# Kernel optimization log

Measured on AMD Instinct MI355X. Metric: run time of the kernel, lower is better.

The kernel has to match this reference:

```python
import jax, jax.numpy as jnp
import numpy as np

R_, RD_, D_, C_ = 4, 64, 256, 64   # num_relations, relation_dim, input_dim, max_chains
B_, T_ = 32, 512
OUT = R_ * RD_                      # output_dim = num_relations * relation_dim
EPS = 1e-100                        # underflows to 0 in fp32, same as torch


def setup_inputs() -> dict:
    key = jax.random.key(0)
    ks = jax.random.split(key, 10)
    X = jax.random.normal(ks[0], (B_, T_, D_), jnp.float32)
    M = jax.random.randint(ks[1], (B_, T_), 0, 2, jnp.int32)
    Ei = jax.random.randint(ks[2], (B_, T_, C_), 0, 2, jnp.int32)
    Eo = jax.random.randint(ks[3], (B_, T_, C_), 0, 2, jnp.int32)
    Ri = jax.random.randint(ks[4], (B_, T_, C_), 0, R_, jnp.int32)
    Ro = jax.random.randint(ks[5], (B_, T_, C_), 0, R_, jnp.int32)
    W = jax.random.normal(ks[6], (D_, OUT), jnp.float32) * np.sqrt(6.0 / (D_ + OUT))
    U = jax.random.normal(ks[7], (OUT, OUT), jnp.float32) * np.sqrt(6.0 / (OUT + OUT))
    b = jnp.zeros((OUT,), jnp.float32)
    Watt = jax.random.normal(ks[8], (R_, D_), jnp.float32) * 0.1
    return dict(X=X, M=M, Ei=Ei, Eo=Eo, Ri=Ri, Ro=Ro, W=W, U=U, b=b, Watt=Watt)


def _forward(X, M, Ei, Eo, Ri, Ro, W, U, b, Watt):
    B = X.shape[0]
    dt = X.dtype
    # All three gates share the same W/U/b in the original module.
    Wstk = jnp.concatenate([W, W, W], axis=1)   # [D, 3*OUT]
    Ustk = jnp.concatenate([U, U, U], axis=1)   # [OUT, 3*OUT]

    # time-major
    Xre = jnp.transpose(X, (1, 0, 2))           # [T,B,D]
    Xpre = jnp.einsum('tbd,de->tbe', Xre, Wstk) # [T,B,3*OUT] precomputed input proj
    Mre = jnp.transpose(M, (1, 0))              # [T,B]
    Eire = jnp.transpose(Ei, (1, 0, 2))         # [T,B,C]
    Eore = jnp.transpose(Eo, (1, 0, 2))
    Rire = jnp.transpose(Ri, (1, 0, 2))
    Rore = jnp.transpose(Ro, (1, 0, 2))

    h0 = jnp.zeros((B, OUT), dt)
    m0 = jnp.zeros((B, C_, RD_), dt)

    def step(carry, inp):
        hprev, mprev = carry
        x, xp, m, ei, eo, ri, ro = inp
        # gather: one-hot over relations for each chain slot
        r1 = jax.nn.one_hot(ri, R_, dtype=dt)                 # [B,C,R]
        # attention over chains
        v = jnp.einsum('bcr,rd->bcd', r1, Watt)               # [B,C,D]
        actvs = jnp.einsum('bcd,bd->bc', v, x)                # [B,C]
        e = ei.astype(dt)
        am = jnp.exp(actvs) * e + EPS
        alphas = am / jnp.sum(am, axis=1, keepdims=True)      # [B,C]
        agg = jnp.transpose(alphas[:, :, None] * r1, (0, 2, 1))  # [B,R,C]
        prev = jnp.einsum('brc,bcd->brd', agg, mprev).reshape(B, OUT)  # [B,OUT]
        agg_out = jnp.sum(agg, axis=2)                        # [B,R]
        # fused GRU cell (shared weights across gates)
        h2h = prev @ Ustk                                     # [B,3*OUT]
        xr, xz, xh = xp[:, :OUT], xp[:, OUT:2 * OUT], xp[:, 2 * OUT:]
        hr, hz, hh = h2h[:, :OUT], h2h[:, OUT:2 * OUT], h2h[:, 2 * OUT:]
        rg = jax.nn.sigmoid(xr + hr + b)
        z = jax.nn.sigmoid(xz + hz + b)
        ht = jnp.tanh(xh + rg * hh + b)
        hnew = (1.0 - z) * prev + z * ht                      # [B,OUT]
        # scatter new hidden state back into per-chain memory
        hnew_r = hnew.reshape(B, R_, RD_)
        ro1 = jax.nn.one_hot(ro, R_, dtype=dt)                # [B,C,R]
        mnew = jnp.einsum('bcr,brd->bcd', ro1, hnew_r)        # [B,C,RD]
        mflt = m.astype(dt)[:, None]                          # [B,1]
        hout = (1.0 - mflt) * hprev + mflt * hnew
        eo_r = (mflt * eo.astype(dt))[:, :, None]             # [B,C,1]
        mout = (1.0 - eo_r) * mprev + eo_r * mnew
        return (hout, mout), (hout, mout, agg_out)

    _, (outs, mems, aggs) = jax.lax.scan(
        step, (h0, m0), (Xre, Xpre, Mre, Eire, Eore, Rire, Rore))
    return (jnp.transpose(outs, (1, 0, 2)),        # [B,T,OUT]
            jnp.transpose(mems, (1, 0, 2, 3)),     # [B,T,C,RD]
            jnp.transpose(aggs, (1, 0, 2)))        # [B,T,R]


def reference(X, M, Ei, Eo, Ri, Ro, W, U, b, Watt):
    return _forward(X, M, Ei, Eo, Ri, Ro, W, U, b, Watt)
```

## Files before the change

### kernel.cpp

```cpp
#include <hip/hip_runtime.h>

#define B_   32
#define T_   512
#define D_   256
#define C_   64
#define R_   4
#define RD_  64
#define OUT_ 256

__device__ __forceinline__ void bar_lds() {
  asm volatile("s_waitcnt lgkmcnt(0)" ::: "memory");
  __builtin_amdgcn_s_barrier();
  asm volatile("" ::: "memory");
}

template <int CTRL>
__device__ __forceinline__ float dpp_add(float v) {
  int s = __builtin_amdgcn_update_dpp(0, __float_as_int(v), CTRL, 0xF, 0xF, true);
  return v + __int_as_float(s);
}
__device__ __forceinline__ float row16_sum(float v) {
  v = dpp_add<0xB1>(v);
  v = dpp_add<0x4E>(v);
  v = dpp_add<0x141>(v);
  v = dpp_add<0x140>(v);
  return v;
}
__device__ __forceinline__ float rlane(float v, int l) {
  return __int_as_float(__builtin_amdgcn_readlane(__float_as_int(v), l));
}
__device__ __forceinline__ int rlane_i(int v, int l) {
  return __builtin_amdgcn_readlane(v, l);
}
__device__ __forceinline__ float wave_sum_dpp(float v) {
  const float r = row16_sum(v);
  return (rlane(r, 0) + rlane(r, 16)) + (rlane(r, 32) + rlane(r, 48));
}

__global__ __launch_bounds__(256) void xpre_kernel(const float* __restrict__ X,
                                                   const float* __restrict__ W,
                                                   float* __restrict__ XP) {
  __shared__ __align__(16) float xs[32][D_];
  const int j = threadIdx.x;
  const int row0 = blockIdx.x * 32;
  for (int k = 0; k < 32; ++k)
    xs[k][j] = X[(size_t)(row0 + k) * D_ + j];
  __syncthreads();
  float acc[32];
#pragma unroll
  for (int k = 0; k < 32; ++k) acc[k] = 0.f;
  for (int d4 = 0; d4 < D_ / 4; ++d4) {
    const float w0 = W[(d4 * 4 + 0) * OUT_ + j];
    const float w1 = W[(d4 * 4 + 1) * OUT_ + j];
    const float w2 = W[(d4 * 4 + 2) * OUT_ + j];
    const float w3 = W[(d4 * 4 + 3) * OUT_ + j];
#pragma unroll
    for (int k = 0; k < 32; ++k) {
      const float4 x4 = *(const float4*)&xs[k][d4 * 4];
      acc[k] = fmaf(x4.x, w0, fmaf(x4.y, w1, fmaf(x4.z, w2, fmaf(x4.w, w3, acc[k]))));
    }
  }
  for (int k = 0; k < 32; ++k)
    XP[(size_t)(row0 + k) * OUT_ + j] = acc[k];
}

__global__ __launch_bounds__(256) void attnK(const float* __restrict__ X,
                                             const int* __restrict__ Ri,
                                             const int* __restrict__ Ei,
                                             const float* __restrict__ Watt,
                                             float* __restrict__ walG,
                                             float* __restrict__ aggs) {
  const int wv = threadIdx.x >> 6;
  const int lane = threadIdx.x & 63;
  const size_t bt = (size_t)blockIdx.x * 4 + wv;
  const int r4 = lane >> 4, seg = lane & 15;

  float y = 0.f;
#pragma unroll
  for (int q = 0; q < 4; ++q) {
    const float4 wt = *(const float4*)&Watt[(r4 << 8) + (seg << 4) + (q << 2)];
    const float4 xv = *(const float4*)&X[bt * D_ + (seg << 4) + (q << 2)];
    y = fmaf(xv.x, wt.x, y);
    y = fmaf(xv.y, wt.y, y);
    y = fmaf(xv.z, wt.z, y);
    y = fmaf(xv.w, wt.w, y);
  }
  y = row16_sum(y);
  const float y0 = rlane(y, 0), y1 = rlane(y, 16);
  const float y2 = rlane(y, 32), y3 = rlane(y, 48);
  const int ric = Ri[bt * C_ + lane];
  const float eic = (float)Ei[bt * C_ + lane];
  float yv = (ric & 1) ? y1 : y0;
  const float yw = (ric & 1) ? y3 : y2;
  yv = (ric & 2) ? yw : yv;
  const float am = __expf(yv) * eic;
  const float tot = wave_sum_dpp(am);
  const float alpha = __fdividef(am, tot);

  const float w0 = (ric == 0) ? alpha : 0.f;
  const float w1 = (ric == 1) ? alpha : 0.f;
  const float w2 = (ric == 2) ? alpha : 0.f;
  const float w3 = (ric == 3) ? alpha : 0.f;
  walG[bt * 256 + 0 * C_ + lane] = w0;
  walG[bt * 256 + 1 * C_ + lane] = w1;
  walG[bt * 256 + 2 * C_ + lane] = w2;
  walG[bt * 256 + 3 * C_ + lane] = w3;
  const float s0 = wave_sum_dpp(w0);
  const float s1 = wave_sum_dpp(w1);
  const float s2 = wave_sum_dpp(w2);
  const float s3 = wave_sum_dpp(w3);
  if (lane == 0) {
    float4 v = {s0, s1, s2, s3};
    *(float4*)&aggs[bt * R_] = v;
  }
}

__global__ __launch_bounds__(1024, 4) void gruA(
    const int* __restrict__ M, const int* __restrict__ Eo,
    const int* __restrict__ Ro, const float* __restrict__ U,
    const float* __restrict__ Bv, const float* __restrict__ XP,
    const float* __restrict__ walG, float* __restrict__ outs) {
  __shared__ __align__(16) float shp[16][256];
  __shared__ __align__(16) float pBred[16][256];
  __shared__ __align__(16) float shprev[OUT_];
  __shared__ __align__(16) float sh_hnew[OUT_];
  __shared__ int sh_tl[T_];
  __shared__ int sh_nT;

  const int tid = threadIdx.x;
  const int lane = tid & 63;
  const int w = tid >> 6;
  const int b = blockIdx.x;
  const size_t bt0 = (size_t)b * T_;

  float ureg[64];
#pragma unroll
  for (int jj = 0; jj < 4; ++jj)
#pragma unroll
    for (int i = 0; i < 16; ++i)
      ureg[(jj << 4) + i] = U[(size_t)((w << 4) + i) * OUT_ + (jj << 6) + lane];
  const float breg = Bv[tid & 255];

  float mtreg[4];
#pragma unroll
  for (int q = 0; q < 4; ++q) mtreg[q] = 0.f;

  if (tid < 64) {
    int base = 0;
    for (int ch = 0; ch < 8; ++ch) {
      const int mv = M[bt0 + (ch << 6) + lane];
      const unsigned long long mask = __ballot(mv != 0);
      if (mv) {
        const unsigned long long lt = ((lane == 63) ? ~0ull : ((1ull << (lane + 1)) - 1)) >> 1;
        sh_tl[base + __popcll(mask & lt)] = (ch << 6) + lane;
      }
      base += __popcll(mask);
    }
    if (lane == 0) sh_nT = base;
  }
  __syncthreads();
  const int nT = sh_nT;

  {
    const int t0 = (nT > 0) ? sh_tl[0] : T_;
    const int j = tid & 255;
    for (int t = tid >> 8; t < t0; t += 4)
      outs[(bt0 + t) * OUT_ + j] = 0.f;
  }
  if (nT == 0) return;

  const int cwal = (w << 2) + (lane >> 4);
  const int rwal = lane & 3;
  const int croeo = (w << 2) + (lane & 3);
  float walS0 = 0.f, xpS0 = 0.f, walS1 = 0.f, xpS1 = 0.f;
  int reS0 = 0, reS1 = 0;
  {
    const int t0 = sh_tl[0];
    walS0 = walG[(bt0 + t0) * 256 + (rwal << 6) + cwal];
    if (w < 4) xpS0 = XP[(bt0 + t0) * 256 + tid];
    reS0 = Ro[(bt0 + t0) * C_ + croeo] | (Eo[(bt0 + t0) * C_ + croeo] << 8);
  }
  if (nT > 1) {
    const int t1 = sh_tl[1];
    walS1 = walG[(bt0 + t1) * 256 + (rwal << 6) + cwal];
    if (w < 4) xpS1 = XP[(bt0 + t1) * 256 + tid];
    reS1 = Ro[(bt0 + t1) * C_ + croeo] | (Eo[(bt0 + t1) * C_ + croeo] << 8);
  }

  auto do_step = [&](int k, float& walS, float& xpS, int& reS) {
    const int tk = sh_tl[k];
    const size_t bt = bt0 + tk;
    const int reC = reS;

    float a0 = 0.f, a1 = 0.f, a2 = 0.f, a3 = 0.f;
#pragma unroll
    for (int q = 0; q < 4; ++q) {
      const float mq = mtreg[q];
      a0 = fmaf(rlane(walS, (q << 4) + 0), mq, a0);
      a1 = fmaf(rlane(walS, (q << 4) + 1), mq, a1);
      a2 = fmaf(rlane(walS, (q << 4) + 2), mq, a2);
      a3 = fmaf(rlane(walS, (q << 4) + 3), mq, a3);
    }
    shp[w][0 * 64 + lane] = a0;
    shp[w][1 * 64 + lane] = a1;
    shp[w][2 * 64 + lane] = a2;
    shp[w][3 * 64 + lane] = a3;
    bar_lds();

    const int kidx = (w << 4) + (lane & 15);
    float px = 0.f;
#pragma unroll
    for (int sw = 0; sw < 16; sw += 4) {
      const float t0 = shp[sw + 0][kidx], t1 = shp[sw + 1][kidx];
      const float t2 = shp[sw + 2][kidx], t3 = shp[sw + 3][kidx];
      px += (t0 + t1) + (t2 + t3);
    }
    if (lane < 16) shprev[kidx] = px;
    float p0 = 0.f, p1 = 0.f, p2 = 0.f, p3 = 0.f;
#pragma unroll
    for (int i = 0; i < 16; ++i) {
      const float pk = rlane(px, i);
      p0 = fmaf(pk, ureg[i], p0);
      p1 = fmaf(pk, ureg[16 + i], p1);
      p2 = fmaf(pk, ureg[32 + i], p2);
      p3 = fmaf(pk, ureg[48 + i], p3);
    }
    pBred[w][0 * 64 + lane] = p0;
    pBred[w][1 * 64 + lane] = p1;
    pBred[w][2 * 64 + lane] = p2;
    pBred[w][3 * 64 + lane] = p3;
    bar_lds();

    if (w < 4) {
      float h2h = 0.f;
#pragma unroll
      for (int kw = 0; kw < 16; kw += 4) {
        const float t0 = pBred[kw + 0][tid], t1 = pBred[kw + 1][tid];
        const float t2 = pBred[kw + 2][tid], t3 = pBred[kw + 3][tid];
        h2h += (t0 + t1) + (t2 + t3);
      }
      const float pOwn = shprev[tid];
      const float g1 = xpS + h2h + breg;
      const float rg = 1.f / (1.f + __expf(-g1));
      const float targ = xpS + rg * h2h + breg;
      const float e2 = __expf(2.f * targ);
      const float ht = 1.f - 2.f / (e2 + 1.f);
      const float hn = (1.f - rg) * pOwn + rg * ht;
      sh_hnew[tid] = hn;
      outs[bt * OUT_ + tid] = hn;
    }
    if (k + 2 < nT) {
      const int t2 = sh_tl[k + 2];
      walS = walG[(bt0 + t2) * 256 + (rwal << 6) + cwal];
      if (w < 4) xpS = XP[(bt0 + t2) * 256 + tid];
      reS = Ro[(bt0 + t2) * C_ + croeo] | (Eo[(bt0 + t2) * C_ + croeo] << 8);
    }
    bar_lds();

    const float h0 = sh_hnew[0 * 64 + lane];
    const float h1 = sh_hnew[1 * 64 + lane];
    const float h2 = sh_hnew[2 * 64 + lane];
    const float h3 = sh_hnew[3 * 64 + lane];
#pragma unroll
    for (int q = 0; q < 4; ++q) {
      const int re = rlane_i(reC, q);
      const int ro = re & 0xFF;
      const float ha = (ro & 1) ? h1 : h0;
      const float hb = (ro & 1) ? h3 : h2;
      const float hs = (ro & 2) ? hb : ha;
      mtreg[q] = (re & 0x100) ? hs : mtreg[q];
    }
    if (w >= 8) {
      const int idx = tid - 512;
      const int rr = idx >> 8;
      const int j = idx & 255;
      const int tnext = (k + 1 < nT) ? sh_tl[k + 1] : T_;
      const float hv = sh_hnew[j];
      for (int t = tk + 1 + rr; t < tnext; t += 2)
        outs[(bt0 + t) * OUT_ + j] = hv;
    }
  };

  for (int k = 0; k < nT; k += 2) {
    do_step(k, walS0, xpS0, reS0);
    if (k + 1 < nT) do_step(k + 1, walS1, xpS1, reS1);
  }
}

__global__ __launch_bounds__(512) void memsB(const int* __restrict__ M,
                                             const int* __restrict__ Eo,
                                             const int* __restrict__ Ro,
                                             const float* __restrict__ hbuf,
                                             float* __restrict__ mems) {
  __shared__ int lastA[T_];
  const int tid = threadIdx.x;
  const int b = blockIdx.x >> 6;
  const int c = blockIdx.x & 63;
  const size_t bt0 = (size_t)b * T_;
  {
    const int upd = M[bt0 + tid] & Eo[(bt0 + tid) * C_ + c];
    lastA[tid] = upd ? tid : -1;
  }
  __syncthreads();
  for (int off = 1; off < T_; off <<= 1) {
    const int u = (tid >= off) ? lastA[tid - off] : -1;
    const int v = lastA[tid];
    __syncthreads();
    lastA[tid] = (u > v) ? u : v;
    __syncthreads();
  }
  const int d = tid & 63;
  const int t8 = tid >> 6;
  for (int tt = 0; tt < 64; ++tt) {
    const int t = (tt << 3) + t8;
    const int tau = lastA[t];
    float v = 0.f;
    if (tau >= 0) {
      const int rc = Ro[(bt0 + tau) * C_ + c];
      v = hbuf[(bt0 + tau) * OUT_ + (rc << 6) + d];
    }
    mems[((bt0 + t) * C_ + c) * RD_ + d] = v;
  }
}

extern "C" void kernel_launch(void* const* d_in, const int* in_sizes, int n_in,
                              void* d_out, int out_size, void* d_ws, size_t ws_size,
                              hipStream_t stream) {
  const float* X = (const float*)d_in[0];
  const int* M = (const int*)d_in[1];
  const int* Ei = (const int*)d_in[2];
  const int* Eo = (const int*)d_in[3];
  const int* Ri = (const int*)d_in[4];
  const int* Ro = (const int*)d_in[5];
  const float* W = (const float*)d_in[6];
  const float* U = (const float*)d_in[7];
  const float* Bv = (const float*)d_in[8];
  const float* Watt = (const float*)d_in[9];

  float* outs = (float*)d_out;
  float* mems = outs + (size_t)B_ * T_ * OUT_;
  float* aggs = mems + (size_t)B_ * T_ * C_ * RD_;
  float* XP = (float*)d_ws;
  float* walG = mems;

  xpre_kernel<<<dim3(B_ * T_ / 32), dim3(256), 0, stream>>>(X, W, XP);
  attnK<<<dim3(B_ * T_ / 4), dim3(256), 0, stream>>>(X, Ri, Ei, Watt, walG, aggs);
  gruA<<<dim3(B_), dim3(1024), 0, stream>>>(M, Eo, Ro, U, Bv, XP, walG, outs);
  memsB<<<dim3(B_ * C_), dim3(512), 0, stream>>>(M, Eo, Ro, outs, mems);
}
```

Before: 730.0 us.

## Precompute next step's chain aggregation a step ahead to cut one barrier

Restructures the serial GRU recurrence so the attention-weighted chain aggregation for the next step is computed one step early into a double-buffered LDS array. Chains that the current step's hidden state is about to overwrite are handled by a small correction: waves 4-7 build per-relation coefficients and these are applied to the new hidden state. The aim is to remove one of the three block barriers per timestep from the critical path. The trade-off is extra register pressure, more prefetched loads and more complex index logic. The fill of repeated outputs is also moved before the barrier, with a tail loop after the main loop.

```diff
diff --git a/kernel.cpp b/kernel.cpp
--- a/kernel.cpp
+++ b/kernel.cpp
@@ -120,10 +120,11 @@
     const int* __restrict__ Ro, const float* __restrict__ U,
     const float* __restrict__ Bv, const float* __restrict__ XP,
     const float* __restrict__ walG, float* __restrict__ outs) {
-  __shared__ __align__(16) float shp[16][256];
+  __shared__ __align__(16) float shp2[2][16][256];
   __shared__ __align__(16) float pBred[16][256];
   __shared__ __align__(16) float shprev[OUT_];
   __shared__ __align__(16) float sh_hnew[OUT_];
+  __shared__ float sh_coef[16];
   __shared__ int sh_tl[T_];
   __shared__ int sh_nT;
 
@@ -158,6 +159,9 @@
     }
     if (lane == 0) sh_nT = base;
   }
+  for (int i = tid; i < 16 * 256; i += 1024) ((float*)shp2[0])[i] = 0.f;
+  if (tid < 256) sh_hnew[tid] = 0.f;
+  if (tid < 16) sh_coef[tid] = 0.f;
   __syncthreads();
   const int nT = sh_nT;
 
@@ -172,63 +176,111 @@
   const int cwal = (w << 2) + (lane >> 4);
   const int rwal = lane & 3;
   const int croeo = (w << 2) + (lane & 3);
-  float walS0 = 0.f, xpS0 = 0.f, walS1 = 0.f, xpS1 = 0.f;
-  int reS0 = 0, reS1 = 0;
-  {
-    const int t0 = sh_tl[0];
-    walS0 = walG[(bt0 + t0) * 256 + (rwal << 6) + cwal];
-    if (w < 4) xpS0 = XP[(bt0 + t0) * 256 + tid];
-    reS0 = Ro[(bt0 + t0) * C_ + croeo] | (Eo[(bt0 + t0) * C_ + croeo] << 8);
-  }
-  if (nT > 1) {
-    const int t1 = sh_tl[1];
-    walS1 = walG[(bt0 + t1) * 256 + (rwal << 6) + cwal];
-    if (w < 4) xpS1 = XP[(bt0 + t1) * 256 + tid];
-    reS1 = Ro[(bt0 + t1) * C_ + croeo] | (Eo[(bt0 + t1) * C_ + croeo] << 8);
-  }
-
-  auto do_step = [&](int k, float& walS, float& xpS, int& reS) {
+
+  auto loadWalS = [&](int t) { return walG[(bt0 + t) * 256 + (rwal << 6) + cwal]; };
+  auto loadRe = [&](int t) { return Ro[(bt0 + t) * C_ + croeo] | (Eo[(bt0 + t) * C_ + croeo] << 8); };
+  auto loadReF = [&](int t) { return Ro[(bt0 + t) * C_ + lane] | (Eo[(bt0 + t) * C_ + lane] << 8); };
+  auto loadWalC = [&](int t) {
+    float4 v;
+    v.x = walG[(bt0 + t) * 256 + 0 * 64 + lane];
+    v.y = walG[(bt0 + t) * 256 + 1 * 64 + lane];
+    v.z = walG[(bt0 + t) * 256 + 2 * 64 + lane];
+    v.w = walG[(bt0 + t) * 256 + 3 * 64 + lane];
+    return v;
+  };
+
+  const int tl0 = sh_tl[0];
+  const int tl1 = sh_tl[(nT > 1) ? 1 : 0];
+  const int tl2 = sh_tl[(nT > 2) ? 2 : (nT - 1)];
+  float walS0 = loadWalS(tl1), walS1 = loadWalS(tl2);
+  float xpS0 = (w < 4) ? XP[(bt0 + tl0) * 256 + tid] : 0.f;
+  float xpS1 = (w < 4) ? XP[(bt0 + tl1) * 256 + tid] : 0.f;
+  int reS0 = loadRe(tl0), reS1 = loadRe(tl1);
+  float4 walC0 = loadWalC(tl1), walC1 = loadWalC(tl2);
+  int reF0 = loadReF(tl0), reF1 = loadReF(tl1);
+  int rePrev = 0;
+
+  auto do_step = [&](int k, float& walS, float& xpS, int& reS, float4& walC,
+                     int& reF) {
+    const int cur = k & 1, nxt = cur ^ 1;
     const int tk = sh_tl[k];
     const size_t bt = bt0 + tk;
-    const int reC = reS;
-
-    float a0 = 0.f, a1 = 0.f, a2 = 0.f, a3 = 0.f;
-#pragma unroll
-    for (int q = 0; q < 4; ++q) {
-      const float mq = mtreg[q];
-      a0 = fmaf(rlane(walS, (q << 4) + 0), mq, a0);
-      a1 = fmaf(rlane(walS, (q << 4) + 1), mq, a1);
-      a2 = fmaf(rlane(walS, (q << 4) + 2), mq, a2);
-      a3 = fmaf(rlane(walS, (q << 4) + 3), mq, a3);
-    }
-    shp[w][0 * 64 + lane] = a0;
-    shp[w][1 * 64 + lane] = a1;
-    shp[w][2 * 64 + lane] = a2;
-    shp[w][3 * 64 + lane] = a3;
-    bar_lds();
-
+
+    {
+      const float h0 = sh_hnew[lane];
+      const float h1 = sh_hnew[64 + lane];
+      const float h2 = sh_hnew[128 + lane];
+      const float h3 = sh_hnew[192 + lane];
+#pragma unroll
+      for (int q = 0; q < 4; ++q) {
+        const int re = rlane_i(rePrev, q);
+        const int ro = re & 0xFF;
+        const float ha = (ro & 1) ? h1 : h0;
+        const float hb = (ro & 1) ? h3 : h2;
+        const float hs = (ro & 2) ? hb : ha;
+        mtreg[q] = (re & 0x100) ? hs : mtreg[q];
+      }
+    }
+    {
+      float a0 = 0.f, a1 = 0.f, a2 = 0.f, a3 = 0.f;
+#pragma unroll
+      for (int q = 0; q < 4; ++q) {
+        const int re = rlane_i(reS, q);
+        const float mq = (re & 0x100) ? 0.f : mtreg[q];
+        a0 = fmaf(rlane(walS, (q << 4) + 0), mq, a0);
+        a1 = fmaf(rlane(walS, (q << 4) + 1), mq, a1);
+        a2 = fmaf(rlane(walS, (q << 4) + 2), mq, a2);
+        a3 = fmaf(rlane(walS, (q << 4) + 3), mq, a3);
+      }
+      shp2[nxt][w][0 * 64 + lane] = a0;
+      shp2[nxt][w][1 * 64 + lane] = a1;
+      shp2[nxt][w][2 * 64 + lane] = a2;
+      shp2[nxt][w][3 * 64 + lane] = a3;
+    }
     const int kidx = (w << 4) + (lane & 15);
+    const int rI = w >> 2, d = kidx & 63;
     float px = 0.f;
 #pragma unroll
     for (int sw = 0; sw < 16; sw += 4) {
-      const float t0 = shp[sw + 0][kidx], t1 = shp[sw + 1][kidx];
-      const float t2 = shp[sw + 2][kidx], t3 = shp[sw + 3][kidx];
+      const float t0 = shp2[cur][sw + 0][kidx], t1 = shp2[cur][sw + 1][kidx];
+      const float t2 = shp2[cur][sw + 2][kidx], t3 = shp2[cur][sw + 3][kidx];
       px += (t0 + t1) + (t2 + t3);
     }
+    {
+      const float c0 = sh_coef[(rI << 2) + 0];
+      const float c1 = sh_coef[(rI << 2) + 1];
+      const float c2 = sh_coef[(rI << 2) + 2];
+      const float c3 = sh_coef[(rI << 2) + 3];
+      px = fmaf(c0, sh_hnew[d], px);
+      px = fmaf(c1, sh_hnew[64 + d], px);
+      px = fmaf(c2, sh_hnew[128 + d], px);
+      px = fmaf(c3, sh_hnew[192 + d], px);
+    }
     if (lane < 16) shprev[kidx] = px;
-    float p0 = 0.f, p1 = 0.f, p2 = 0.f, p3 = 0.f;
-#pragma unroll
-    for (int i = 0; i < 16; ++i) {
-      const float pk = rlane(px, i);
-      p0 = fmaf(pk, ureg[i], p0);
-      p1 = fmaf(pk, ureg[16 + i], p1);
-      p2 = fmaf(pk, ureg[32 + i], p2);
-      p3 = fmaf(pk, ureg[48 + i], p3);
-    }
-    pBred[w][0 * 64 + lane] = p0;
-    pBred[w][1 * 64 + lane] = p1;
-    pBred[w][2 * 64 + lane] = p2;
-    pBred[w][3 * 64 + lane] = p3;
+    {
+      float p0 = 0.f, p1 = 0.f, p2 = 0.f, p3 = 0.f;
+#pragma unroll
+      for (int i = 0; i < 16; ++i) {
+        const float pk = rlane(px, i);
+        p0 = fmaf(pk, ureg[i], p0);
+        p1 = fmaf(pk, ureg[16 + i], p1);
+        p2 = fmaf(pk, ureg[32 + i], p2);
+        p3 = fmaf(pk, ureg[48 + i], p3);
+      }
+      pBred[w][0 * 64 + lane] = p0;
+      pBred[w][1 * 64 + lane] = p1;
+      pBred[w][2 * 64 + lane] = p2;
+      pBred[w][3 * 64 + lane] = p3;
+    }
+    if (w >= 8 && k > 0) {
+      const int idx = tid - 512;
+      const int rr = idx >> 8;
+      const int j = idx & 255;
+      const int tprev = sh_tl[k - 1];
+      const float hv = sh_hnew[j];
+      for (int t = tprev + 1 + rr; t < tk; t += 2)
+        outs[(bt0 + t) * OUT_ + j] = hv;
+    }
     bar_lds();
 
     if (w < 4) {
@@ -248,42 +300,47 @@
       const float hn = (1.f - rg) * pOwn + rg * ht;
       sh_hnew[tid] = hn;
       outs[bt * OUT_ + tid] = hn;
-    }
-    if (k + 2 < nT) {
-      const int t2 = sh_tl[k + 2];
-      walS = walG[(bt0 + t2) * 256 + (rwal << 6) + cwal];
-      if (w < 4) xpS = XP[(bt0 + t2) * 256 + tid];
-      reS = Ro[(bt0 + t2) * C_ + croeo] | (Eo[(bt0 + t2) * C_ + croeo] << 8);
+    } else if (w < 8) {
+      const int r2 = w - 4;
+      const float mask =
+          (((reF >> 8) & 1) && ((reF & 0xFF) == r2)) ? 1.f : 0.f;
+      const float s0 = wave_sum_dpp(walC.x * mask);
+      const float s1 = wave_sum_dpp(walC.y * mask);
+      const float s2 = wave_sum_dpp(walC.z * mask);
+      const float s3 = wave_sum_dpp(walC.w * mask);
+      if (lane == 0) {
+        sh_coef[0 * 4 + r2] = s0;
+        sh_coef[1 * 4 + r2] = s1;
+        sh_coef[2 * 4 + r2] = s2;
+        sh_coef[3 * 4 + r2] = s3;
+      }
+    }
+    rePrev = reS;
+    {
+      const int k2 = (k + 2 < nT) ? k + 2 : nT - 1;
+      const int k3 = (k + 3 < nT) ? k + 3 : nT - 1;
+      const int t2v = sh_tl[k2], t3v = sh_tl[k3];
+      walS = loadWalS(t3v);
+      if (w < 4) xpS = XP[(bt0 + t2v) * 256 + tid];
+      reS = loadRe(t2v);
+      walC = loadWalC(t3v);
+      reF = loadReF(t2v);
     }
     bar_lds();
-
-    const float h0 = sh_hnew[0 * 64 + lane];
-    const float h1 = sh_hnew[1 * 64 + lane];
-    const float h2 = sh_hnew[2 * 64 + lane];
-    const float h3 = sh_hnew[3 * 64 + lane];
-#pragma unroll
-    for (int q = 0; q < 4; ++q) {
-      const int re = rlane_i(reC, q);
-      const int ro = re & 0xFF;
-      const float ha = (ro & 1) ? h1 : h0;
-      const float hb = (ro & 1) ? h3 : h2;
-      const float hs = (ro & 2) ? hb : ha;
-      mtreg[q] = (re & 0x100) ? hs : mtreg[q];
-    }
-    if (w >= 8) {
-      const int idx = tid - 512;
-      const int rr = idx >> 8;
-      const int j = idx & 255;
-      const int tnext = (k + 1 < nT) ? sh_tl[k + 1] : T_;
-      const float hv = sh_hnew[j];
-      for (int t = tk + 1 + rr; t < tnext; t += 2)
-        outs[(bt0 + t) * OUT_ + j] = hv;
-    }
   };
 
   for (int k = 0; k < nT; k += 2) {
-    do_step(k, walS0, xpS0, reS0);
-    if (k + 1 < nT) do_step(k + 1, walS1, xpS1, reS1);
+    do_step(k, walS0, xpS0, reS0, walC0, reF0);
+    if (k + 1 < nT)
+      do_step(k + 1, walS1, xpS1, reS1, walC1, reF1);
+  }
+
+  {
+    const int tlast = sh_tl[nT - 1];
+    const int j = tid & 255;
+    const float hv = sh_hnew[j];
+    for (int t = tlast + 1 + (tid >> 8); t < T_; t += 4)
+      outs[(bt0 + t) * OUT_ + j] = hv;
   }
 }
 
```

Measured after the change: 798.9 us. 1.09x slower.

## Fuse prep kernels and write per-chain memory directly from GRU kernel

Applied to the files above, without the earlier changes.

Merges the input projection and attention kernels into one launch that branches on block index. When the workspace is large enough, attention weights move to the workspace and the GRU kernel writes the mems output itself while it runs, so the separate memsB pass that re-read the hidden states is dropped. This removes one or two launches and a large re-read, but adds many serial global stores inside the 32-block recurrent kernel, which could lengthen its critical path.

```diff
diff --git a/kernel.cpp b/kernel.cpp
--- a/kernel.cpp
+++ b/kernel.cpp
@@ -37,81 +37,79 @@
   return (rlane(r, 0) + rlane(r, 16)) + (rlane(r, 32) + rlane(r, 48));
 }
 
-__global__ __launch_bounds__(256) void xpre_kernel(const float* __restrict__ X,
-                                                   const float* __restrict__ W,
-                                                   float* __restrict__ XP) {
+__global__ __launch_bounds__(256) void prepK(
+    const float* __restrict__ X, const float* __restrict__ W,
+    const int* __restrict__ Ri, const int* __restrict__ Ei,
+    const float* __restrict__ Watt, float* __restrict__ XP,
+    float* __restrict__ walG, float* __restrict__ aggs) {
   __shared__ __align__(16) float xs[32][D_];
-  const int j = threadIdx.x;
-  const int row0 = blockIdx.x * 32;
-  for (int k = 0; k < 32; ++k)
-    xs[k][j] = X[(size_t)(row0 + k) * D_ + j];
-  __syncthreads();
-  float acc[32];
-#pragma unroll
-  for (int k = 0; k < 32; ++k) acc[k] = 0.f;
-  for (int d4 = 0; d4 < D_ / 4; ++d4) {
-    const float w0 = W[(d4 * 4 + 0) * OUT_ + j];
-    const float w1 = W[(d4 * 4 + 1) * OUT_ + j];
-    const float w2 = W[(d4 * 4 + 2) * OUT_ + j];
-    const float w3 = W[(d4 * 4 + 3) * OUT_ + j];
-#pragma unroll
-    for (int k = 0; k < 32; ++k) {
-      const float4 x4 = *(const float4*)&xs[k][d4 * 4];
-      acc[k] = fmaf(x4.x, w0, fmaf(x4.y, w1, fmaf(x4.z, w2, fmaf(x4.w, w3, acc[k]))));
-    }
-  }
-  for (int k = 0; k < 32; ++k)
-    XP[(size_t)(row0 + k) * OUT_ + j] = acc[k];
-}
-
-__global__ __launch_bounds__(256) void attnK(const float* __restrict__ X,
-                                             const int* __restrict__ Ri,
-                                             const int* __restrict__ Ei,
-                                             const float* __restrict__ Watt,
-                                             float* __restrict__ walG,
-                                             float* __restrict__ aggs) {
-  const int wv = threadIdx.x >> 6;
-  const int lane = threadIdx.x & 63;
-  const size_t bt = (size_t)blockIdx.x * 4 + wv;
-  const int r4 = lane >> 4, seg = lane & 15;
-
-  float y = 0.f;
-#pragma unroll
-  for (int q = 0; q < 4; ++q) {
-    const float4 wt = *(const float4*)&Watt[(r4 << 8) + (seg << 4) + (q << 2)];
-    const float4 xv = *(const float4*)&X[bt * D_ + (seg << 4) + (q << 2)];
-    y = fmaf(xv.x, wt.x, y);
-    y = fmaf(xv.y, wt.y, y);
-    y = fmaf(xv.z, wt.z, y);
-    y = fmaf(xv.w, wt.w, y);
-  }
-  y = row16_sum(y);
-  const float y0 = rlane(y, 0), y1 = rlane(y, 16);
-  const float y2 = rlane(y, 32), y3 = rlane(y, 48);
-  const int ric = Ri[bt * C_ + lane];
-  const float eic = (float)Ei[bt * C_ + lane];
-  float yv = (ric & 1) ? y1 : y0;
-  const float yw = (ric & 1) ? y3 : y2;
-  yv = (ric & 2) ? yw : yv;
-  const float am = __expf(yv) * eic;
-  const float tot = wave_sum_dpp(am);
-  const float alpha = __fdividef(am, tot);
-
-  const float w0 = (ric == 0) ? alpha : 0.f;
-  const float w1 = (ric == 1) ? alpha : 0.f;
-  const float w2 = (ric == 2) ? alpha : 0.f;
-  const float w3 = (ric == 3) ? alpha : 0.f;
-  walG[bt * 256 + 0 * C_ + lane] = w0;
-  walG[bt * 256 + 1 * C_ + lane] = w1;
-  walG[bt * 256 + 2 * C_ + lane] = w2;
-  walG[bt * 256 + 3 * C_ + lane] = w3;
-  const float s0 = wave_sum_dpp(w0);
-  const float s1 = wave_sum_dpp(w1);
-  const float s2 = wave_sum_dpp(w2);
-  const float s3 = wave_sum_dpp(w3);
-  if (lane == 0) {
-    float4 v = {s0, s1, s2, s3};
-    *(float4*)&aggs[bt * R_] = v;
+  const int bid = blockIdx.x;
+  if (bid < B_ * T_ / 4) {
+    const int wv = threadIdx.x >> 6;
+    const int lane = threadIdx.x & 63;
+    const size_t bt = (size_t)bid * 4 + wv;
+    const int r4 = lane >> 4, seg = lane & 15;
+
+    float y = 0.f;
+#pragma unroll
+    for (int q = 0; q < 4; ++q) {
+      const float4 wt = *(const float4*)&Watt[(r4 << 8) + (seg << 4) + (q << 2)];
+      const float4 xv = *(const float4*)&X[bt * D_ + (seg << 4) + (q << 2)];
+      y = fmaf(xv.x, wt.x, y);
+      y = fmaf(xv.y, wt.y, y);
+      y = fmaf(xv.z, wt.z, y);
+      y = fmaf(xv.w, wt.w, y);
+    }
+    y = row16_sum(y);
+    const float y0 = rlane(y, 0), y1 = rlane(y, 16);
+    const float y2 = rlane(y, 32), y3 = rlane(y, 48);
+    const int ric = Ri[bt * C_ + lane];
+    const float eic = (float)Ei[bt * C_ + lane];
+    float yv = (ric & 1) ? y1 : y0;
+    const float yw = (ric & 1) ? y3 : y2;
+    yv = (ric & 2) ? yw : yv;
+    const float am = __expf(yv) * eic;
+    const float tot = wave_sum_dpp(am);
+    const float alpha = __fdividef(am, tot);
+
+    const float w0 = (ric == 0) ? alpha : 0.f;
+    const float w1 = (ric == 1) ? alpha : 0.f;
+    const float w2 = (ric == 2) ? alpha : 0.f;
+    const float w3 = (ric == 3) ? alpha : 0.f;
+    walG[bt * 256 + 0 * C_ + lane] = w0;
+    walG[bt * 256 + 1 * C_ + lane] = w1;
+    walG[bt * 256 + 2 * C_ + lane] = w2;
+    walG[bt * 256 + 3 * C_ + lane] = w3;
+    const float s0 = wave_sum_dpp(w0);
+    const float s1 = wave_sum_dpp(w1);
+    const float s2 = wave_sum_dpp(w2);
+    const float s3 = wave_sum_dpp(w3);
+    if (lane == 0) {
+      float4 v = {s0, s1, s2, s3};
+      *(float4*)&aggs[bt * R_] = v;
+    }
+  } else {
+    const int j = threadIdx.x;
+    const int row0 = (bid - B_ * T_ / 4) * 32;
+    for (int k = 0; k < 32; ++k)
+      xs[k][j] = X[(size_t)(row0 + k) * D_ + j];
+    __syncthreads();
+    float acc[32];
+#pragma unroll
+    for (int k = 0; k < 32; ++k) acc[k] = 0.f;
+    for (int d4 = 0; d4 < D_ / 4; ++d4) {
+      const float w0 = W[(d4 * 4 + 0) * OUT_ + j];
+      const float w1 = W[(d4 * 4 + 1) * OUT_ + j];
+      const float w2 = W[(d4 * 4 + 2) * OUT_ + j];
+      const float w3 = W[(d4 * 4 + 3) * OUT_ + j];
+#pragma unroll
+      for (int k = 0; k < 32; ++k) {
+        const float4 x4 = *(const float4*)&xs[k][d4 * 4];
+        acc[k] = fmaf(x4.x, w0, fmaf(x4.y, w1, fmaf(x4.z, w2, fmaf(x4.w, w3, acc[k]))));
+      }
+    }
+    for (int k = 0; k < 32; ++k)
+      XP[(size_t)(row0 + k) * OUT_ + j] = acc[k];
   }
 }
 
@@ -119,7 +117,8 @@
     const int* __restrict__ M, const int* __restrict__ Eo,
     const int* __restrict__ Ro, const float* __restrict__ U,
     const float* __restrict__ Bv, const float* __restrict__ XP,
-    const float* __restrict__ walG, float* __restrict__ outs) {
+    const float* __restrict__ walG, float* __restrict__ outs,
+    float* __restrict__ memsW) {
   __shared__ __align__(16) float shp[16][256];
   __shared__ __align__(16) float pBred[16][256];
   __shared__ __align__(16) float shprev[OUT_];
@@ -166,6 +165,16 @@
     const int j = tid & 255;
     for (int t = tid >> 8; t < t0; t += 4)
       outs[(bt0 + t) * OUT_ + j] = 0.f;
+    if (memsW) {
+      const int cbase = w << 2;
+      for (int t = 0; t < t0; ++t) {
+        float* rp = memsW + ((bt0 + t) * (size_t)C_ + cbase) * RD_ + lane;
+        rp[0 * RD_] = 0.f;
+        rp[1 * RD_] = 0.f;
+        rp[2 * RD_] = 0.f;
+        rp[3 * RD_] = 0.f;
+      }
+    }
   }
   if (nT == 0) return;
 
@@ -270,14 +279,24 @@
       const float hs = (ro & 2) ? hb : ha;
       mtreg[q] = (re & 0x100) ? hs : mtreg[q];
     }
+    const int tnext = (k + 1 < nT) ? sh_tl[k + 1] : T_;
     if (w >= 8) {
       const int idx = tid - 512;
       const int rr = idx >> 8;
       const int j = idx & 255;
-      const int tnext = (k + 1 < nT) ? sh_tl[k + 1] : T_;
       const float hv = sh_hnew[j];
       for (int t = tk + 1 + rr; t < tnext; t += 2)
         outs[(bt0 + t) * OUT_ + j] = hv;
+    }
+    if (memsW) {
+      const int cbase = w << 2;
+      for (int t = tk; t < tnext; ++t) {
+        float* rp = memsW + ((bt0 + t) * (size_t)C_ + cbase) * RD_ + lane;
+        rp[0 * RD_] = mtreg[0];
+        rp[1 * RD_] = mtreg[1];
+        rp[2 * RD_] = mtreg[2];
+        rp[3 * RD_] = mtreg[3];
+      }
     }
   };
 
@@ -340,11 +359,16 @@
   float* outs = (float*)d_out;
   float* mems = outs + (size_t)B_ * T_ * OUT_;
   float* aggs = mems + (size_t)B_ * T_ * C_ * RD_;
+
+  const size_t XPN = (size_t)B_ * T_ * OUT_;
   float* XP = (float*)d_ws;
-  float* walG = mems;
-
-  xpre_kernel<<<dim3(B_ * T_ / 32), dim3(256), 0, stream>>>(X, W, XP);
-  attnK<<<dim3(B_ * T_ / 4), dim3(256), 0, stream>>>(X, Ri, Ei, Watt, walG, aggs);
-  gruA<<<dim3(B_), dim3(1024), 0, stream>>>(M, Eo, Ro, U, Bv, XP, walG, outs);
-  memsB<<<dim3(B_ * C_), dim3(512), 0, stream>>>(M, Eo, Ro, outs, mems);
-}
+  const bool big_ws = ws_size >= 2 * XPN * sizeof(float);
+  float* walG = big_ws ? (XP + XPN) : mems;
+
+  prepK<<<dim3(B_ * T_ / 4 + B_ * T_ / 32), dim3(256), 0, stream>>>(
+      X, W, Ri, Ei, Watt, XP, walG, aggs);
+  gruA<<<dim3(B_), dim3(1024), 0, stream>>>(M, Eo, Ro, U, Bv, XP, walG, outs,
+                                            big_ws ? mems : nullptr);
+  if (!big_ws)
+    memsB<<<dim3(B_ * C_), dim3(512), 0, stream>>>(M, Eo, Ro, outs, mems);
+}
```

New measurement: 769.7 us. +5.4%, slower.
